# Kernel optimization log

Measured on AMD Instinct MI355X. Metric: run time of the kernel, lower is better.

## Reference

```python
import jax, jax.numpy as jnp
import numpy as np

V, N, D, C = 3, 4096, 512, 10
PSI = 0.7
CE_SCALE = 0.1


def setup_inputs() -> dict:
    key = jax.random.key(0)
    ks = jax.random.split(key, 10)
    X = jax.random.normal(ks[0], (V, N, D), jnp.float32)
    # sparse-ish symmetric binary adjacency per view (dense storage, as in source)
    A = (jax.random.uniform(ks[1], (V, N, N)) < 0.01).astype(jnp.float32)
    A = jnp.maximum(A, jnp.swapaxes(A, 1, 2))
    # ce_scale * Dirichlet(alpha=ones(C)) samples, one per (view, node)
    consensus = CE_SCALE * jax.random.dirichlet(ks[2], jnp.ones((C,), jnp.float32), (V, N)).astype(jnp.float32)
    W_mlp = jax.random.normal(ks[3], (V, D, C), jnp.float32) * 0.05
    b_mlp = jnp.zeros((V, C), jnp.float32)
    W1 = jax.random.normal(ks[4], (V, D, D), jnp.float32) * 0.05
    b1 = jnp.zeros((V, D), jnp.float32)
    W2 = jax.random.normal(ks[5], (V, D, C), jnp.float32) * 0.05
    b2 = jnp.zeros((V, C), jnp.float32)
    return {"X": X, "A": A, "consensus": consensus, "W_mlp": W_mlp, "b_mlp": b_mlp,
            "W1": W1, "b1": b1, "W2": W2, "b2": b2}


def _gcn_norm(A):
    # A: [V, N, N].  A_hat = A + I;  A_norm = D^{-1/2} A_hat D^{-1/2}
    A_hat = A + jnp.eye(A.shape[-1], dtype=A.dtype)
    dinv = 1.0 / jnp.sqrt(jnp.sum(A_hat, axis=-1))          # [V, N]
    return dinv[:, :, None] * A_hat * dinv[:, None, :]


def reference(X, A, consensus, W_mlp, b_mlp, W1, b1, W2, b2):
    # --- EvidenceCollector (single Linear -> Softplus; dropout is eval-identity) ---
    mlp = jax.nn.softplus(jnp.einsum('vnd,vdc->vnc', X, W_mlp) + b_mlp[:, None, :])
    # --- GCN: softplus(gcn2(gcn1(X, A), A)) ---
    A_norm = _gcn_norm(A)                                    # [V, N, N]
    h = jnp.einsum('vij,vjd->vid', A_norm, X)
    h = jnp.einsum('vnd,vde->vne', h, W1) + b1[:, None, :]   # gcn1 linear
    h = jnp.einsum('vij,vjc->vic', A_norm, h)
    gcn = jax.nn.softplus(jnp.einsum('vnd,vdc->vnc', h, W2) + b2[:, None, :])
    E = consensus + mlp + gcn                                # evidences, [V, N, C]

    # --- create_complete_graph: mean cosine similarity per view-pair (i<j) ---
    En = E / jnp.clip(jnp.linalg.norm(E, axis=-1, keepdims=True), 1e-8)
    S = jnp.einsum('inc,jnc->ij', En, En) / E.shape[1]       # [V, V] mean cos-sim
    mask = jnp.triu(jnp.ones((V, V), bool), k=1)             # edges (i, j), i<j
    max_sim = jnp.max(jnp.where(mask, S, -jnp.inf))
    thr = PSI * max_sim
    w = jnp.where(mask & (S > thr), S, 0.0)                  # thresholded weights

    # --- mrf_aggregate: per-source-row softmax over its edges, weighted sum ---
    logits = jnp.where(mask, w, -1e30)
    m = jnp.max(logits, axis=1, keepdims=True)
    e = jnp.exp(logits - m) * mask                           # zero for non-edges
    p = e / jnp.clip(jnp.sum(e, axis=1, keepdims=True), 1e-30)  # empty rows -> 0
    # sum_{i,j>i} p[i,j] * (E[j] + E[i])
    agg = jnp.einsum('ij,jnc->nc', p, E) + jnp.einsum('i,inc->nc', jnp.sum(p, axis=1), E)
    agg = agg / (2.0 * V)
    return (E, agg)
```

## Files before the change

kernel.cpp:

```cpp
#include <hip/hip_runtime.h>
#include <stdint.h>
#include <stddef.h>

#define VV 3
#define NN 4096
#define DD 512
#define CC 10

typedef unsigned short bf16_t;
typedef __attribute__((ext_vector_type(8))) short bf16x8;
typedef __attribute__((ext_vector_type(4))) float f32x4;

#define MFMA16 __builtin_amdgcn_mfma_f32_16x16x32_bf16

__device__ __forceinline__ float bf2f(unsigned u) {
  union { unsigned u; float f; } c; c.u = u << 16; return c.f;
}
__device__ __forceinline__ bf16_t f2bf(float f) {
  union { float f; unsigned u; } c; c.f = f;
  unsigned r = (c.u + 0x7FFFu + ((c.u >> 16) & 1u)) >> 16;
  return (bf16_t)r;
}
__device__ __forceinline__ float splus(float x) {
  float ax = fabsf(x);
  return fmaxf(x, 0.0f) + log1pf(expf(-ax));
}

__global__ __launch_bounds__(256) void k_prep(const float* __restrict__ A,
    const float* __restrict__ W1, const float* __restrict__ b1,
    const float* __restrict__ W2, const float* __restrict__ W_mlp,
    unsigned long long* __restrict__ mask, float* __restrict__ dinv,
    bf16_t* __restrict__ Wc_t, float* __restrict__ bp, bf16_t* __restrict__ Wm_t)
{
  int t = threadIdx.x;
  int w = t >> 6, lane = t & 63;
  if (blockIdx.x < VV * NN / 4) {
    size_t row = (size_t)blockIdx.x * 4 + w;
    const f32x4* r4 = (const f32x4*)(A + row * NN);
    unsigned long long myw = 0ull;
#pragma unroll 8
    for (int it = 0; it < 16; ++it) {
      f32x4 x = __builtin_nontemporal_load(r4 + it * 64 + lane);
      unsigned long long q0 = __ballot(x[0] != 0.0f);
      unsigned long long q1 = __ballot(x[1] != 0.0f);
      unsigned long long q2 = __ballot(x[2] != 0.0f);
      unsigned long long q3 = __ballot(x[3] != 0.0f);
      if ((lane >> 2) == it) {
        int k = lane & 3;
        myw = (k == 0) ? q0 : (k == 1) ? q1 : (k == 2) ? q2 : q3;
      }
    }
    mask[row * 64 + lane] = myw;
    int pc = __popcll(myw);
#pragma unroll
    for (int s = 32; s; s >>= 1) pc += __shfl_xor(pc, s);
    if (lane == 0) dinv[row] = 1.0f / sqrtf((float)(pc + 1));
  } else if (blockIdx.x < VV * NN / 4 + 385) {
    int wid = (blockIdx.x - VV * NN / 4) * 4 + w;
    if (wid >= VV * 513) return;
    int v = wid / 513, dd2 = wid % 513;
    const float* w2 = W2 + (size_t)v * DD * CC;
    const float* src = (dd2 < DD) ? (W1 + ((size_t)v * DD + dd2) * DD) : (b1 + (size_t)v * DD);
    float acc[CC];
#pragma unroll
    for (int c = 0; c < CC; ++c) acc[c] = 0.f;
    for (int it = 0; it < 8; ++it) {
      float wv = src[it * 64 + lane];
      const float* w2r = w2 + (size_t)(it * 64 + lane) * CC;
#pragma unroll
      for (int c = 0; c < CC; ++c) acc[c] += wv * w2r[c];
    }
#pragma unroll
    for (int c = 0; c < CC; ++c) {
#pragma unroll
      for (int s = 32; s; s >>= 1) acc[c] += __shfl_xor(acc[c], s);
    }
    if (lane == 0) {
      if (dd2 < DD) {
#pragma unroll
        for (int c = 0; c < CC; ++c) Wc_t[((size_t)v * 16 + c) * DD + dd2] = f2bf(acc[c]);
#pragma unroll
        for (int c = CC; c < 16; ++c) Wc_t[((size_t)v * 16 + c) * DD + dd2] = 0;
      } else {
#pragma unroll
        for (int c = 0; c < CC; ++c) bp[v * CC + c] = acc[c];
      }
    }
  } else {
    int idx = (blockIdx.x - (VV * NN / 4 + 385)) * 256 + t;
    if (idx >= VV * DD) return;
    int v = idx / DD, d = idx % DD;
#pragma unroll
    for (int c = 0; c < CC; ++c)
      Wm_t[((size_t)v * 16 + c) * DD + d] = f2bf(W_mlp[((size_t)v * DD + d) * CC + c]);
#pragma unroll
    for (int c = CC; c < 16; ++c) Wm_t[((size_t)v * 16 + c) * DD + d] = 0;
  }
}

__global__ __launch_bounds__(256) void k_zs(
    const float* __restrict__ X,
    const bf16_t* __restrict__ Wc_t, const bf16_t* __restrict__ Wm_t,
    const float* __restrict__ b_mlp, const float* __restrict__ consensus,
    const float* __restrict__ dinv,
    unsigned* __restrict__ Ps1p, float* __restrict__ E)
{
  __shared__ bf16_t Bc[16 * 520];
  __shared__ bf16_t Bm[16 * 520];
  int v = blockIdx.y;
  int t = threadIdx.x;
  {
    int r = t & 15, ch = t >> 4;
    const bf16_t* sc = Wc_t + (size_t)v * 16 * DD + (size_t)r * DD + ch * 32;
    const bf16_t* sm = Wm_t + (size_t)v * 16 * DD + (size_t)r * DD + ch * 32;
    bf16_t* dc = &Bc[r * 520 + ch * 32];
    bf16_t* dm = &Bm[r * 520 + ch * 32];
#pragma unroll
    for (int q = 0; q < 4; ++q) {
      *(bf16x8*)(dc + q * 8) = *(const bf16x8*)(sc + q * 8);
      *(bf16x8*)(dm + q * 8) = *(const bf16x8*)(sm + q * 8);
    }
  }
  __syncthreads();
  int w = t >> 6, lane = t & 63;
  int fl = lane & 15, fh = lane >> 4;
  int r0 = blockIdx.x * 64 + w * 16;
  const float* Xrow = X + ((size_t)v * NN + r0 + fl) * DD;
  f32x4 aP = {0.f, 0.f, 0.f, 0.f}, aM = {0.f, 0.f, 0.f, 0.f};
#pragma unroll
  for (int k = 0; k < 16; ++k) {
    float4 x0 = *(const float4*)(Xrow + k * 32 + fh * 8);
    float4 x1 = *(const float4*)(Xrow + k * 32 + fh * 8 + 4);
    bf16x8 a = { (short)f2bf(x0.x), (short)f2bf(x0.y), (short)f2bf(x0.z), (short)f2bf(x0.w),
                 (short)f2bf(x1.x), (short)f2bf(x1.y), (short)f2bf(x1.z), (short)f2bf(x1.w) };
    bf16x8 b1v = *(const bf16x8*)(&Bc[fl * 520 + k * 32 + fh * 8]);
    aP = MFMA16(a, b1v, aP, 0, 0, 0);
    bf16x8 b2v = *(const bf16x8*)(&Bm[fl * 520 + k * 32 + fh * 8]);
    aM = MFMA16(a, b2v, aM, 0, 0, 0);
  }
  float bmv = (fl < CC) ? b_mlp[v * CC + fl] : 0.f;
#pragma unroll
  for (int g = 0; g < 4; ++g) {
    int j = r0 + fh * 4 + g;
    float dj = dinv[(size_t)v * NN + j];
    float val = aP[g] * dj;
    float part = __shfl_xor(val, 1);
    if (((fl & 1) == 0) && fl < CC) {
      unsigned pw = (unsigned)f2bf(val) | ((unsigned)f2bf(part) << 16);
      Ps1p[((size_t)v * 5 + (fl >> 1)) * NN + j] = pw;
    }
    if (fl < CC) {
      size_t ad = ((size_t)v * NN + j) * CC + fl;
      E[ad] = consensus[ad] + splus(aM[g] + bmv);
    }
  }
}

#define SPMM_PROLOG(SRC_) \
  __shared__ unsigned PsL[5 * NN];   \
  int v = blockIdx.y; \
  int t = threadIdx.x; \
  { \
    const uint4* src_ = (const uint4*)((SRC_) + (size_t)v * 5 * NN); \
    uint4* dst_ = (uint4*)PsL; \
    _Pragma("unroll") \
    for (int q = 0; q < 20; ++q) dst_[q * 256 + t] = src_[q * 256 + t]; \
  } \
  __syncthreads(); \
  int w = t >> 6, g = (t >> 3) & 7, s = t & 7; \
  int i = blockIdx.x * 32 + w * 8 + g; \
  const unsigned long long* mrow = mask + ((size_t)v * NN + i) * 64; \
  float acc[CC]; \
  _Pragma("unroll") \
  for (int c = 0; c < CC; ++c) acc[c] = 0.f; \
  _Pragma("unroll") \
  for (int it = 0; it < 8; ++it) { \
    int wi = it * 8 + s; \
    unsigned long long bits = mrow[wi]; \
    int jb = (wi >> 2) * 256 + (wi & 3); \
    while (bits) { \
      int b = __builtin_ctzll(bits); \
      bits &= bits - 1; \
      int j = jb + (b << 2); \
      _Pragma("unroll") \
      for (int c2 = 0; c2 < 5; ++c2) { \
        unsigned pw = PsL[c2 * NN + j]; \
        acc[2 * c2]     += bf2f(pw & 0xFFFFu); \
        acc[2 * c2 + 1] += bf2f(pw >> 16); \
      } \
    } \
  } \
  _Pragma("unroll") \
  for (int c = 0; c < CC; ++c) { \
    acc[c] += __shfl_xor(acc[c], 1); \
    acc[c] += __shfl_xor(acc[c], 2); \
    acc[c] += __shfl_xor(acc[c], 4); \
  }

__global__ __launch_bounds__(256) void k_spmm1(
    const unsigned long long* __restrict__ mask, const unsigned* __restrict__ Ps1p,
    const float* __restrict__ bp, const float* __restrict__ dinv,
    unsigned* __restrict__ P2p)
{
  SPMM_PROLOG(Ps1p)
  if (s == 0) {
    float di = dinv[(size_t)v * NN + i];
#pragma unroll
    for (int c2 = 0; c2 < 5; ++c2) {
      unsigned pw = PsL[c2 * NN + i];
      acc[2 * c2]     += bf2f(pw & 0xFFFFu);
      acc[2 * c2 + 1] += bf2f(pw >> 16);
    }
#pragma unroll
    for (int c2 = 0; c2 < 5; ++c2) {
      float lo = di * (di * acc[2 * c2]     + bp[v * CC + 2 * c2]);
      float hi = di * (di * acc[2 * c2 + 1] + bp[v * CC + 2 * c2 + 1]);
      P2p[((size_t)v * 5 + c2) * NN + i] = (unsigned)f2bf(lo) | ((unsigned)f2bf(hi) << 16);
    }
  }
}

__global__ __launch_bounds__(256) void k_spmm2(
    const unsigned long long* __restrict__ mask, const unsigned* __restrict__ P2p,
    const float* __restrict__ b2, const float* __restrict__ dinv,
    float* __restrict__ E)
{
  SPMM_PROLOG(P2p)
  if (s == 0) {
    float di = dinv[(size_t)v * NN + i];
#pragma unroll
    for (int c2 = 0; c2 < 5; ++c2) {
      unsigned pw = PsL[c2 * NN + i];
      acc[2 * c2]     += bf2f(pw & 0xFFFFu);
      acc[2 * c2 + 1] += bf2f(pw >> 16);
    }
    float* Eo = E + ((size_t)v * NN + i) * CC;
#pragma unroll
    for (int c = 0; c < CC; ++c)
      Eo[c] = Eo[c] + splus(di * acc[c] + b2[v * CC + c]);
  }
}

__global__ __launch_bounds__(256) void k_tail(const float* __restrict__ E,
    float* __restrict__ partial, unsigned* __restrict__ barcnt,
    float* __restrict__ agg)
{
  __shared__ float sm[3][256];
  int t = threadIdx.x;
  int bid = blockIdx.x;
  if (bid < 16) {
    int n = bid * 256 + t;
    float e0[CC], e1[CC], e2[CC];
#pragma unroll
    for (int c = 0; c < CC; ++c) {
      e0[c] = E[(size_t)(0 * NN + n) * CC + c];
      e1[c] = E[(size_t)(1 * NN + n) * CC + c];
      e2[c] = E[(size_t)(2 * NN + n) * CC + c];
    }
    float n0 = 0, n1 = 0, n2 = 0, d01 = 0, d02 = 0, d12 = 0;
#pragma unroll
    for (int c = 0; c < CC; ++c) { n0 += e0[c]*e0[c]; n1 += e1[c]*e1[c]; n2 += e2[c]*e2[c]; }
    float i0 = 1.0f / fmaxf(sqrtf(n0), 1e-8f);
    float i1 = 1.0f / fmaxf(sqrtf(n1), 1e-8f);
    float i2 = 1.0f / fmaxf(sqrtf(n2), 1e-8f);
#pragma unroll
    for (int c = 0; c < CC; ++c) { d01 += e0[c]*e1[c]; d02 += e0[c]*e2[c]; d12 += e1[c]*e2[c]; }
    sm[0][t] = d01 * i0 * i1;
    sm[1][t] = d02 * i0 * i2;
    sm[2][t] = d12 * i1 * i2;
    __syncthreads();
    for (int s = 128; s; s >>= 1) {
      if (t < s) { sm[0][t] += sm[0][t+s]; sm[1][t] += sm[1][t+s]; sm[2][t] += sm[2][t+s]; }
      __syncthreads();
    }
    if (t == 0) {
      partial[bid * 3 + 0] = sm[0][0];
      partial[bid * 3 + 1] = sm[1][0];
      partial[bid * 3 + 2] = sm[2][0];
    }
  }
  __syncthreads();
  if (t == 0) {
    __builtin_amdgcn_fence(__ATOMIC_RELEASE, "agent");
    __hip_atomic_fetch_add(barcnt, 1u, __ATOMIC_RELAXED, __HIP_MEMORY_SCOPE_AGENT);
    while (__hip_atomic_load(barcnt, __ATOMIC_RELAXED, __HIP_MEMORY_SCOPE_AGENT) < 160u)
      __builtin_amdgcn_s_sleep(8);
    __builtin_amdgcn_fence(__ATOMIC_ACQUIRE, "agent");
  }
  __syncthreads();
  float S01 = 0, S02 = 0, S12 = 0;
  for (int b = 0; b < 16; ++b) {
    S01 += partial[b * 3 + 0];
    S02 += partial[b * 3 + 1];
    S12 += partial[b * 3 + 2];
  }
  S01 /= (float)NN; S02 /= (float)NN; S12 /= (float)NN;
  float mx = fmaxf(S01, fmaxf(S02, S12));
  float thr = 0.7f * mx;
  float w01 = (S01 > thr) ? S01 : 0.f;
  float w02 = (S02 > thr) ? S02 : 0.f;
  float m0 = fmaxf(w01, w02);
  float e01 = expf(w01 - m0), e02 = expf(w02 - m0);
  float s0 = e01 + e02;
  float p01 = e01 / s0, p02 = e02 / s0;
  float p12 = 1.0f;
  float c0 = (p01 + p02) / 6.0f;
  float c1 = (p12 + p01) / 6.0f;
  float c2 = (p02 + p12) / 6.0f;
  int idx = bid * 256 + t;
  agg[idx] = c0 * E[idx] + c1 * E[NN * CC + idx] + c2 * E[2 * NN * CC + idx];
}

extern "C" void kernel_launch(void* const* d_in, const int* in_sizes, int n_in,
                              void* d_out, int out_size, void* d_ws, size_t ws_size,
                              hipStream_t stream)
{
  (void)in_sizes; (void)n_in; (void)out_size;
  const float* X         = (const float*)d_in[0];
  const float* A         = (const float*)d_in[1];
  const float* consensus = (const float*)d_in[2];
  const float* W_mlp     = (const float*)d_in[3];
  const float* b_mlp     = (const float*)d_in[4];
  const float* W1        = (const float*)d_in[5];
  const float* b1        = (const float*)d_in[6];
  const float* W2        = (const float*)d_in[7];
  const float* b2        = (const float*)d_in[8];
  float* Eout = (float*)d_out;
  float* aggout = Eout + (size_t)VV * NN * CC;

  char* ws = (char*)d_ws;
  size_t off = 0;
  auto alloc = [&](size_t b) { char* p = ws + off; off += (b + 255) & ~(size_t)255; return p; };
  unsigned long long* mask = (unsigned long long*)alloc((size_t)VV * NN * 64 * 8);
  bf16_t* Wc_t  = (bf16_t*)alloc((size_t)VV * 16 * DD * 2);
  bf16_t* Wm_t  = (bf16_t*)alloc((size_t)VV * 16 * DD * 2);
  float*  bp    = (float*) alloc((size_t)VV * CC * 4);
  float*  dinv  = (float*) alloc((size_t)VV * NN * 4);
  unsigned* Ps1p = (unsigned*)alloc((size_t)VV * 5 * NN * 4);
  unsigned* P2p  = (unsigned*)alloc((size_t)VV * 5 * NN * 4);
  float*  partial = (float*)alloc(16 * 3 * 4);
  unsigned* barcnt = (unsigned*)alloc(256);
  if (off > ws_size) return;

  hipMemsetAsync(barcnt, 0, 4, stream);
  k_prep <<<VV * NN / 4 + 385 + 6, 256, 0, stream>>>(A, W1, b1, W2, W_mlp,
                                                     mask, dinv, Wc_t, bp, Wm_t);
  k_zs   <<<dim3(NN / 64, VV), 256, 0, stream>>>(X, Wc_t, Wm_t, b_mlp, consensus,
                                                 dinv, Ps1p, Eout);
  k_spmm1<<<dim3(NN / 32, VV), 256, 0, stream>>>(mask, Ps1p, bp, dinv, P2p);
  k_spmm2<<<dim3(NN / 32, VV), 256, 0, stream>>>(mask, P2p, b2, dinv, Eout);
  k_tail <<<160, 256, 0, stream>>>(Eout, partial, barcnt, aggout);
}
```

Measured before the change: 97.15 us.

## Fuse all stages into one cooperative persistent kernel with grid barriers

Replaces five separate launches with one cooperative kernel of 512 blocks that runs the stages prep, projection, two SpMM passes, similarity and aggregation, separated by atomic grid barriers. The intent is to remove inter-kernel launch gaps. The SpMM gathers now read directly from a node-major padded P layout (8 words per node) in global memory instead of staging the whole per-view P array into LDS. The adjacency scan is spread over fewer blocks, each handling 6 rows per wave, and no longer uses nontemporal loads. The risks are lower parallelism in the 50 MB adjacency scan, barrier spin cost, and uncached gather traffic. If the cooperative launch fails, the code falls back to six separate launches.

```diff
diff --git a/kernel.cpp b/kernel.cpp
--- a/kernel.cpp
+++ b/kernel.cpp
@@ -6,6 +6,7 @@
 #define NN 4096
 #define DD 512
 #define CC 10
+#define NBLK 512
 
 typedef unsigned short bf16_t;
 typedef __attribute__((ext_vector_type(8))) short bf16x8;
@@ -26,21 +27,73 @@
   return fmaxf(x, 0.0f) + log1pf(expf(-ax));
 }
 
-__global__ __launch_bounds__(256) void k_prep(const float* __restrict__ A,
-    const float* __restrict__ W1, const float* __restrict__ b1,
-    const float* __restrict__ W2, const float* __restrict__ W_mlp,
+__device__ __forceinline__ void gsync(unsigned* cnt, unsigned target, int t) {
+  __syncthreads();
+  if (t == 0) {
+    __builtin_amdgcn_fence(__ATOMIC_RELEASE, "agent");
+    __hip_atomic_fetch_add(cnt, 1u, __ATOMIC_RELAXED, __HIP_MEMORY_SCOPE_AGENT);
+    while (__hip_atomic_load(cnt, __ATOMIC_RELAXED, __HIP_MEMORY_SCOPE_AGENT) < target)
+      __builtin_amdgcn_s_sleep(16);
+    __builtin_amdgcn_fence(__ATOMIC_ACQUIRE, "agent");
+  }
+  __syncthreads();
+}
+
+__device__ __forceinline__ void dev_prep(int bid, int t,
+    const float* __restrict__ A, const float* __restrict__ W1,
+    const float* __restrict__ b1, const float* __restrict__ W2,
+    const float* __restrict__ W_mlp,
     unsigned long long* __restrict__ mask, float* __restrict__ dinv,
     bf16_t* __restrict__ Wc_t, float* __restrict__ bp, bf16_t* __restrict__ Wm_t)
 {
-  int t = threadIdx.x;
   int w = t >> 6, lane = t & 63;
-  if (blockIdx.x < VV * NN / 4) {
-    size_t row = (size_t)blockIdx.x * 4 + w;
+  int gw = bid * 4 + w;
+  int gt = bid * 256 + t;
+  if (gt < VV * DD) {
+    int v = gt / DD, d = gt - v * DD;
+#pragma unroll
+    for (int c = 0; c < CC; ++c)
+      Wm_t[((size_t)v * 16 + c) * DD + d] = f2bf(W_mlp[((size_t)v * DD + d) * CC + c]);
+#pragma unroll
+    for (int c = CC; c < 16; ++c) Wm_t[((size_t)v * 16 + c) * DD + d] = 0;
+  }
+  if (gw < VV * 513) {
+    int v = gw / 513, dd2 = gw % 513;
+    const float* w2 = W2 + (size_t)v * DD * CC;
+    const float* src = (dd2 < DD) ? (W1 + ((size_t)v * DD + dd2) * DD) : (b1 + (size_t)v * DD);
+    float acc[CC];
+#pragma unroll
+    for (int c = 0; c < CC; ++c) acc[c] = 0.f;
+    for (int it = 0; it < 8; ++it) {
+      float wv = src[it * 64 + lane];
+      const float* w2r = w2 + (size_t)(it * 64 + lane) * CC;
+#pragma unroll
+      for (int c = 0; c < CC; ++c) acc[c] += wv * w2r[c];
+    }
+#pragma unroll
+    for (int c = 0; c < CC; ++c) {
+#pragma unroll
+      for (int s = 32; s; s >>= 1) acc[c] += __shfl_xor(acc[c], s);
+    }
+    if (lane == 0) {
+      if (dd2 < DD) {
+#pragma unroll
+        for (int c = 0; c < CC; ++c) Wc_t[((size_t)v * 16 + c) * DD + dd2] = f2bf(acc[c]);
+#pragma unroll
+        for (int c = CC; c < 16; ++c) Wc_t[((size_t)v * 16 + c) * DD + dd2] = 0;
+      } else {
+#pragma unroll
+        for (int c = 0; c < CC; ++c) bp[v * CC + c] = acc[c];
+      }
+    }
+  }
+  for (int p = 0; p < 6; ++p) {
+    size_t row = (size_t)gw * 6 + p;
     const f32x4* r4 = (const f32x4*)(A + row * NN);
     unsigned long long myw = 0ull;
-#pragma unroll 8
+#pragma unroll 4
     for (int it = 0; it < 16; ++it) {
-      f32x4 x = __builtin_nontemporal_load(r4 + it * 64 + lane);
+      f32x4 x = r4[it * 64 + lane];
       unsigned long long q0 = __ballot(x[0] != 0.0f);
       unsigned long long q1 = __ballot(x[1] != 0.0f);
       unsigned long long q2 = __ballot(x[2] != 0.0f);
@@ -55,76 +108,33 @@
 #pragma unroll
     for (int s = 32; s; s >>= 1) pc += __shfl_xor(pc, s);
     if (lane == 0) dinv[row] = 1.0f / sqrtf((float)(pc + 1));
-  } else if (blockIdx.x < VV * NN / 4 + 385) {
-    int wid = (blockIdx.x - VV * NN / 4) * 4 + w;
-    if (wid >= VV * 513) return;
-    int v = wid / 513, dd2 = wid % 513;
-    const float* w2 = W2 + (size_t)v * DD * CC;
-    const float* src = (dd2 < DD) ? (W1 + ((size_t)v * DD + dd2) * DD) : (b1 + (size_t)v * DD);
-    float acc[CC];
-#pragma unroll
-    for (int c = 0; c < CC; ++c) acc[c] = 0.f;
-    for (int it = 0; it < 8; ++it) {
-      float wv = src[it * 64 + lane];
-      const float* w2r = w2 + (size_t)(it * 64 + lane) * CC;
-#pragma unroll
-      for (int c = 0; c < CC; ++c) acc[c] += wv * w2r[c];
-    }
-#pragma unroll
-    for (int c = 0; c < CC; ++c) {
-#pragma unroll
-      for (int s = 32; s; s >>= 1) acc[c] += __shfl_xor(acc[c], s);
-    }
-    if (lane == 0) {
-      if (dd2 < DD) {
-#pragma unroll
-        for (int c = 0; c < CC; ++c) Wc_t[((size_t)v * 16 + c) * DD + dd2] = f2bf(acc[c]);
-#pragma unroll
-        for (int c = CC; c < 16; ++c) Wc_t[((size_t)v * 16 + c) * DD + dd2] = 0;
-      } else {
-#pragma unroll
-        for (int c = 0; c < CC; ++c) bp[v * CC + c] = acc[c];
-      }
-    }
-  } else {
-    int idx = (blockIdx.x - (VV * NN / 4 + 385)) * 256 + t;
-    if (idx >= VV * DD) return;
-    int v = idx / DD, d = idx % DD;
-#pragma unroll
-    for (int c = 0; c < CC; ++c)
-      Wm_t[((size_t)v * 16 + c) * DD + d] = f2bf(W_mlp[((size_t)v * DD + d) * CC + c]);
-#pragma unroll
-    for (int c = CC; c < 16; ++c) Wm_t[((size_t)v * 16 + c) * DD + d] = 0;
-  }
-}
-
-__global__ __launch_bounds__(256) void k_zs(
-    const float* __restrict__ X,
-    const bf16_t* __restrict__ Wc_t, const bf16_t* __restrict__ Wm_t,
-    const float* __restrict__ b_mlp, const float* __restrict__ consensus,
-    const float* __restrict__ dinv,
+  }
+}
+
+__device__ __forceinline__ void dev_zs(int bid, int t, bf16_t* Bc, bf16_t* Bm,
+    const float* __restrict__ X, const bf16_t* __restrict__ Wc_t,
+    const bf16_t* __restrict__ Wm_t, const float* __restrict__ b_mlp,
+    const float* __restrict__ consensus, const float* __restrict__ dinv,
     unsigned* __restrict__ Ps1p, float* __restrict__ E)
 {
-  __shared__ bf16_t Bc[16 * 520];
-  __shared__ bf16_t Bm[16 * 520];
-  int v = blockIdx.y;
-  int t = threadIdx.x;
+  if (bid >= 192) return;
+  int v = bid / 64, xb = bid % 64;
   {
     int r = t & 15, ch = t >> 4;
     const bf16_t* sc = Wc_t + (size_t)v * 16 * DD + (size_t)r * DD + ch * 32;
-    const bf16_t* sm = Wm_t + (size_t)v * 16 * DD + (size_t)r * DD + ch * 32;
+    const bf16_t* sm2 = Wm_t + (size_t)v * 16 * DD + (size_t)r * DD + ch * 32;
     bf16_t* dc = &Bc[r * 520 + ch * 32];
     bf16_t* dm = &Bm[r * 520 + ch * 32];
 #pragma unroll
     for (int q = 0; q < 4; ++q) {
       *(bf16x8*)(dc + q * 8) = *(const bf16x8*)(sc + q * 8);
-      *(bf16x8*)(dm + q * 8) = *(const bf16x8*)(sm + q * 8);
+      *(bf16x8*)(dm + q * 8) = *(const bf16x8*)(sm2 + q * 8);
     }
   }
   __syncthreads();
   int w = t >> 6, lane = t & 63;
   int fl = lane & 15, fh = lane >> 4;
-  int r0 = blockIdx.x * 64 + w * 16;
+  int r0 = xb * 64 + w * 16;
   const float* Xrow = X + ((size_t)v * NN + r0 + fl) * DD;
   f32x4 aP = {0.f, 0.f, 0.f, 0.f}, aM = {0.f, 0.f, 0.f, 0.f};
 #pragma unroll
@@ -147,7 +157,7 @@
     float part = __shfl_xor(val, 1);
     if (((fl & 1) == 0) && fl < CC) {
       unsigned pw = (unsigned)f2bf(val) | ((unsigned)f2bf(part) << 16);
-      Ps1p[((size_t)v * 5 + (fl >> 1)) * NN + j] = pw;
+      Ps1p[((size_t)v * NN + j) * 8 + (fl >> 1)] = pw;
     }
     if (fl < CC) {
       size_t ad = ((size_t)v * NN + j) * CC + fl;
@@ -156,138 +166,114 @@
   }
 }
 
-#define SPMM_PROLOG(SRC_) \
-  __shared__ unsigned PsL[5 * NN];   \
-  int v = blockIdx.y; \
-  int t = threadIdx.x; \
-  { \
-    const uint4* src_ = (const uint4*)((SRC_) + (size_t)v * 5 * NN); \
-    uint4* dst_ = (uint4*)PsL; \
-    _Pragma("unroll") \
-    for (int q = 0; q < 20; ++q) dst_[q * 256 + t] = src_[q * 256 + t]; \
-  } \
-  __syncthreads(); \
-  int w = t >> 6, g = (t >> 3) & 7, s = t & 7; \
-  int i = blockIdx.x * 32 + w * 8 + g; \
-  const unsigned long long* mrow = mask + ((size_t)v * NN + i) * 64; \
-  float acc[CC]; \
-  _Pragma("unroll") \
-  for (int c = 0; c < CC; ++c) acc[c] = 0.f; \
-  _Pragma("unroll") \
-  for (int it = 0; it < 8; ++it) { \
-    int wi = it * 8 + s; \
-    unsigned long long bits = mrow[wi]; \
-    int jb = (wi >> 2) * 256 + (wi & 3); \
-    while (bits) { \
-      int b = __builtin_ctzll(bits); \
-      bits &= bits - 1; \
-      int j = jb + (b << 2); \
-      _Pragma("unroll") \
-      for (int c2 = 0; c2 < 5; ++c2) { \
-        unsigned pw = PsL[c2 * NN + j]; \
-        acc[2 * c2]     += bf2f(pw & 0xFFFFu); \
-        acc[2 * c2 + 1] += bf2f(pw >> 16); \
-      } \
-    } \
-  } \
-  _Pragma("unroll") \
-  for (int c = 0; c < CC; ++c) { \
-    acc[c] += __shfl_xor(acc[c], 1); \
-    acc[c] += __shfl_xor(acc[c], 2); \
-    acc[c] += __shfl_xor(acc[c], 4); \
-  }
-
-__global__ __launch_bounds__(256) void k_spmm1(
-    const unsigned long long* __restrict__ mask, const unsigned* __restrict__ Ps1p,
-    const float* __restrict__ bp, const float* __restrict__ dinv,
-    unsigned* __restrict__ P2p)
-{
-  SPMM_PROLOG(Ps1p)
-  if (s == 0) {
-    float di = dinv[(size_t)v * NN + i];
-#pragma unroll
-    for (int c2 = 0; c2 < 5; ++c2) {
-      unsigned pw = PsL[c2 * NN + i];
-      acc[2 * c2]     += bf2f(pw & 0xFFFFu);
-      acc[2 * c2 + 1] += bf2f(pw >> 16);
-    }
-#pragma unroll
-    for (int c2 = 0; c2 < 5; ++c2) {
-      float lo = di * (di * acc[2 * c2]     + bp[v * CC + 2 * c2]);
-      float hi = di * (di * acc[2 * c2 + 1] + bp[v * CC + 2 * c2 + 1]);
-      P2p[((size_t)v * 5 + c2) * NN + i] = (unsigned)f2bf(lo) | ((unsigned)f2bf(hi) << 16);
-    }
-  }
-}
-
-__global__ __launch_bounds__(256) void k_spmm2(
-    const unsigned long long* __restrict__ mask, const unsigned* __restrict__ P2p,
-    const float* __restrict__ b2, const float* __restrict__ dinv,
-    float* __restrict__ E)
-{
-  SPMM_PROLOG(P2p)
-  if (s == 0) {
-    float di = dinv[(size_t)v * NN + i];
-#pragma unroll
-    for (int c2 = 0; c2 < 5; ++c2) {
-      unsigned pw = PsL[c2 * NN + i];
-      acc[2 * c2]     += bf2f(pw & 0xFFFFu);
-      acc[2 * c2 + 1] += bf2f(pw >> 16);
-    }
-    float* Eo = E + ((size_t)v * NN + i) * CC;
-#pragma unroll
-    for (int c = 0; c < CC; ++c)
-      Eo[c] = Eo[c] + splus(di * acc[c] + b2[v * CC + c]);
-  }
-}
-
-__global__ __launch_bounds__(256) void k_tail(const float* __restrict__ E,
-    float* __restrict__ partial, unsigned* __restrict__ barcnt,
+template<int PASS>
+__device__ __forceinline__ void dev_spmm(int bid, int t,
+    const unsigned long long* __restrict__ mask, const unsigned* __restrict__ Pin,
+    const float* __restrict__ bvec, const float* __restrict__ dinv,
+    unsigned* __restrict__ Pout, float* __restrict__ E)
+{
+  int gid = (bid * 256 + t) >> 3;
+  int s8 = t & 7;
+  if (gid >= VV * NN) return;
+  int v = gid >> 12;
+  const unsigned long long* mrow = mask + (size_t)gid * 64;
+  const unsigned* Pv = Pin + (size_t)v * NN * 8;
+  float acc[CC];
+#pragma unroll
+  for (int c = 0; c < CC; ++c) acc[c] = 0.f;
+#pragma unroll
+  for (int it = 0; it < 8; ++it) {
+    int wi = it * 8 + s8;
+    unsigned long long bits = mrow[wi];
+    int jb = (wi >> 2) * 256 + (wi & 3);
+    while (bits) {
+      int b = __builtin_ctzll(bits);
+      bits &= bits - 1;
+      int j = jb + (b << 2);
+      const unsigned* pw = Pv + (size_t)j * 8;
+      uint4 p0 = *(const uint4*)pw;
+      unsigned p4 = pw[4];
+      acc[0] += bf2f(p0.x & 0xFFFFu); acc[1] += bf2f(p0.x >> 16);
+      acc[2] += bf2f(p0.y & 0xFFFFu); acc[3] += bf2f(p0.y >> 16);
+      acc[4] += bf2f(p0.z & 0xFFFFu); acc[5] += bf2f(p0.z >> 16);
+      acc[6] += bf2f(p0.w & 0xFFFFu); acc[7] += bf2f(p0.w >> 16);
+      acc[8] += bf2f(p4 & 0xFFFFu);   acc[9] += bf2f(p4 >> 16);
+    }
+  }
+#pragma unroll
+  for (int c = 0; c < CC; ++c) {
+    acc[c] += __shfl_xor(acc[c], 1);
+    acc[c] += __shfl_xor(acc[c], 2);
+    acc[c] += __shfl_xor(acc[c], 4);
+  }
+  if (s8 == 0) {
+    const unsigned* ps = Pin + (size_t)gid * 8;
+    uint4 p0 = *(const uint4*)ps;
+    unsigned p4 = ps[4];
+    acc[0] += bf2f(p0.x & 0xFFFFu); acc[1] += bf2f(p0.x >> 16);
+    acc[2] += bf2f(p0.y & 0xFFFFu); acc[3] += bf2f(p0.y >> 16);
+    acc[4] += bf2f(p0.z & 0xFFFFu); acc[5] += bf2f(p0.z >> 16);
+    acc[6] += bf2f(p0.w & 0xFFFFu); acc[7] += bf2f(p0.w >> 16);
+    acc[8] += bf2f(p4 & 0xFFFFu);   acc[9] += bf2f(p4 >> 16);
+    float di = dinv[gid];
+    if (PASS == 1) {
+#pragma unroll
+      for (int c2 = 0; c2 < 5; ++c2) {
+        float lo = di * (di * acc[2 * c2]     + bvec[v * CC + 2 * c2]);
+        float hi = di * (di * acc[2 * c2 + 1] + bvec[v * CC + 2 * c2 + 1]);
+        Pout[(size_t)gid * 8 + c2] = (unsigned)f2bf(lo) | ((unsigned)f2bf(hi) << 16);
+      }
+    } else {
+      float* Eo = E + (size_t)gid * CC;
+#pragma unroll
+      for (int c = 0; c < CC; ++c)
+        Eo[c] = Eo[c] + splus(di * acc[c] + bvec[v * CC + c]);
+    }
+  }
+}
+
+__device__ __forceinline__ void dev_sim(int bid, int t, float* sm,
+    const float* __restrict__ E, float* __restrict__ partial)
+{
+  if (bid >= 16) return;
+  int n = bid * 256 + t;
+  float e0[CC], e1[CC], e2[CC];
+#pragma unroll
+  for (int c = 0; c < CC; ++c) {
+    e0[c] = E[(size_t)(0 * NN + n) * CC + c];
+    e1[c] = E[(size_t)(1 * NN + n) * CC + c];
+    e2[c] = E[(size_t)(2 * NN + n) * CC + c];
+  }
+  float n0 = 0, n1 = 0, n2 = 0, d01 = 0, d02 = 0, d12 = 0;
+#pragma unroll
+  for (int c = 0; c < CC; ++c) { n0 += e0[c]*e0[c]; n1 += e1[c]*e1[c]; n2 += e2[c]*e2[c]; }
+  float i0 = 1.0f / fmaxf(sqrtf(n0), 1e-8f);
+  float i1 = 1.0f / fmaxf(sqrtf(n1), 1e-8f);
+  float i2 = 1.0f / fmaxf(sqrtf(n2), 1e-8f);
+#pragma unroll
+  for (int c = 0; c < CC; ++c) { d01 += e0[c]*e1[c]; d02 += e0[c]*e2[c]; d12 += e1[c]*e2[c]; }
+  sm[0 * 256 + t] = d01 * i0 * i1;
+  sm[1 * 256 + t] = d02 * i0 * i2;
+  sm[2 * 256 + t] = d12 * i1 * i2;
+  __syncthreads();
+  for (int s = 128; s; s >>= 1) {
+    if (t < s) {
+      sm[0*256+t] += sm[0*256+t+s]; sm[1*256+t] += sm[1*256+t+s]; sm[2*256+t] += sm[2*256+t+s];
+    }
+    __syncthreads();
+  }
+  if (t == 0) {
+    partial[bid * 3 + 0] = sm[0];
+    partial[bid * 3 + 1] = sm[256];
+    partial[bid * 3 + 2] = sm[512];
+  }
+}
+
+__device__ __forceinline__ void dev_agg(int bid, int t,
+    const float* __restrict__ E, const float* __restrict__ partial,
     float* __restrict__ agg)
 {
-  __shared__ float sm[3][256];
-  int t = threadIdx.x;
-  int bid = blockIdx.x;
-  if (bid < 16) {
-    int n = bid * 256 + t;
-    float e0[CC], e1[CC], e2[CC];
-#pragma unroll
-    for (int c = 0; c < CC; ++c) {
-      e0[c] = E[(size_t)(0 * NN + n) * CC + c];
-      e1[c] = E[(size_t)(1 * NN + n) * CC + c];
-      e2[c] = E[(size_t)(2 * NN + n) * CC + c];
-    }
-    float n0 = 0, n1 = 0, n2 = 0, d01 = 0, d02 = 0, d12 = 0;
-#pragma unroll
-    for (int c = 0; c < CC; ++c) { n0 += e0[c]*e0[c]; n1 += e1[c]*e1[c]; n2 += e2[c]*e2[c]; }
-    float i0 = 1.0f / fmaxf(sqrtf(n0), 1e-8f);
-    float i1 = 1.0f / fmaxf(sqrtf(n1), 1e-8f);
-    float i2 = 1.0f / fmaxf(sqrtf(n2), 1e-8f);
-#pragma unroll
-    for (int c = 0; c < CC; ++c) { d01 += e0[c]*e1[c]; d02 += e0[c]*e2[c]; d12 += e1[c]*e2[c]; }
-    sm[0][t] = d01 * i0 * i1;
-    sm[1][t] = d02 * i0 * i2;
-    sm[2][t] = d12 * i1 * i2;
-    __syncthreads();
-    for (int s = 128; s; s >>= 1) {
-      if (t < s) { sm[0][t] += sm[0][t+s]; sm[1][t] += sm[1][t+s]; sm[2][t] += sm[2][t+s]; }
-      __syncthreads();
-    }
-    if (t == 0) {
-      partial[bid * 3 + 0] = sm[0][0];
-      partial[bid * 3 + 1] = sm[1][0];
-      partial[bid * 3 + 2] = sm[2][0];
-    }
-  }
-  __syncthreads();
-  if (t == 0) {
-    __builtin_amdgcn_fence(__ATOMIC_RELEASE, "agent");
-    __hip_atomic_fetch_add(barcnt, 1u, __ATOMIC_RELAXED, __HIP_MEMORY_SCOPE_AGENT);
-    while (__hip_atomic_load(barcnt, __ATOMIC_RELAXED, __HIP_MEMORY_SCOPE_AGENT) < 160u)
-      __builtin_amdgcn_s_sleep(8);
-    __builtin_amdgcn_fence(__ATOMIC_ACQUIRE, "agent");
-  }
-  __syncthreads();
+  if (bid >= 160) return;
   float S01 = 0, S02 = 0, S12 = 0;
   for (int b = 0; b < 16; ++b) {
     S01 += partial[b * 3 + 0];
@@ -311,6 +297,55 @@
   agg[idx] = c0 * E[idx] + c1 * E[NN * CC + idx] + c2 * E[2 * NN * CC + idx];
 }
 
+__global__ __launch_bounds__(256) void k_all(
+    const float* __restrict__ A, const float* __restrict__ X,
+    const float* __restrict__ consensus,
+    const float* __restrict__ W_mlp, const float* __restrict__ b_mlp,
+    const float* __restrict__ W1, const float* __restrict__ b1,
+    const float* __restrict__ W2, const float* __restrict__ b2,
+    unsigned long long* __restrict__ mask,
+    bf16_t* __restrict__ Wc_t, bf16_t* __restrict__ Wm_t, float* __restrict__ bp,
+    float* __restrict__ dinv, unsigned* __restrict__ Ps1p,
+    unsigned* __restrict__ P2p, float* __restrict__ partial,
+    unsigned* __restrict__ barcnt, float* __restrict__ E, float* __restrict__ agg)
+{
+  __shared__ bf16_t Bc[16 * 520];
+  __shared__ bf16_t Bm[16 * 520];
+  __shared__ float sm[3 * 256];
+  int t = threadIdx.x, bid = blockIdx.x;
+  dev_prep(bid, t, A, W1, b1, W2, W_mlp, mask, dinv, Wc_t, bp, Wm_t);
+  gsync(barcnt, 1 * NBLK, t);
+  dev_zs(bid, t, Bc, Bm, X, Wc_t, Wm_t, b_mlp, consensus, dinv, Ps1p, E);
+  gsync(barcnt, 2 * NBLK, t);
+  dev_spmm<1>(bid, t, mask, Ps1p, bp, dinv, P2p, E);
+  gsync(barcnt, 3 * NBLK, t);
+  dev_spmm<2>(bid, t, mask, P2p, b2, dinv, (unsigned*)nullptr, E);
+  gsync(barcnt, 4 * NBLK, t);
+  dev_sim(bid, t, sm, E, partial);
+  gsync(barcnt, 5 * NBLK, t);
+  dev_agg(bid, t, E, partial, agg);
+}
+
+__global__ __launch_bounds__(256) void k_one(int ph,
+    const float* A, const float* X, const float* consensus,
+    const float* W_mlp, const float* b_mlp,
+    const float* W1, const float* b1, const float* W2, const float* b2,
+    unsigned long long* mask, bf16_t* Wc_t, bf16_t* Wm_t, float* bp,
+    float* dinv, unsigned* Ps1p, unsigned* P2p, float* partial,
+    float* E, float* agg)
+{
+  __shared__ bf16_t Bc[16 * 520];
+  __shared__ bf16_t Bm[16 * 520];
+  __shared__ float sm[3 * 256];
+  int t = threadIdx.x, bid = blockIdx.x;
+  if (ph == 0)      dev_prep(bid, t, A, W1, b1, W2, W_mlp, mask, dinv, Wc_t, bp, Wm_t);
+  else if (ph == 1) dev_zs(bid, t, Bc, Bm, X, Wc_t, Wm_t, b_mlp, consensus, dinv, Ps1p, E);
+  else if (ph == 2) dev_spmm<1>(bid, t, mask, Ps1p, bp, dinv, P2p, E);
+  else if (ph == 3) dev_spmm<2>(bid, t, mask, P2p, b2, dinv, (unsigned*)nullptr, E);
+  else if (ph == 4) dev_sim(bid, t, sm, E, partial);
+  else              dev_agg(bid, t, E, partial, agg);
+}
+
 extern "C" void kernel_launch(void* const* d_in, const int* in_sizes, int n_in,
                               void* d_out, int out_size, void* d_ws, size_t ws_size,
                               hipStream_t stream)
@@ -336,18 +371,35 @@
   bf16_t* Wm_t  = (bf16_t*)alloc((size_t)VV * 16 * DD * 2);
   float*  bp    = (float*) alloc((size_t)VV * CC * 4);
   float*  dinv  = (float*) alloc((size_t)VV * NN * 4);
-  unsigned* Ps1p = (unsigned*)alloc((size_t)VV * 5 * NN * 4);
-  unsigned* P2p  = (unsigned*)alloc((size_t)VV * 5 * NN * 4);
+  unsigned* Ps1p = (unsigned*)alloc((size_t)VV * NN * 8 * 4);
+  unsigned* P2p  = (unsigned*)alloc((size_t)VV * NN * 8 * 4);
   float*  partial = (float*)alloc(16 * 3 * 4);
   unsigned* barcnt = (unsigned*)alloc(256);
   if (off > ws_size) return;
 
   hipMemsetAsync(barcnt, 0, 4, stream);
-  k_prep <<<VV * NN / 4 + 385 + 6, 256, 0, stream>>>(A, W1, b1, W2, W_mlp,
-                                                     mask, dinv, Wc_t, bp, Wm_t);
-  k_zs   <<<dim3(NN / 64, VV), 256, 0, stream>>>(X, Wc_t, Wm_t, b_mlp, consensus,
-                                                 dinv, Ps1p, Eout);
-  k_spmm1<<<dim3(NN / 32, VV), 256, 0, stream>>>(mask, Ps1p, bp, dinv, P2p);
-  k_spmm2<<<dim3(NN / 32, VV), 256, 0, stream>>>(mask, P2p, b2, dinv, Eout);
-  k_tail <<<160, 256, 0, stream>>>(Eout, partial, barcnt, aggout);
-}
+
+  void* kargs[] = {
+    (void*)&A, (void*)&X, (void*)&consensus, (void*)&W_mlp, (void*)&b_mlp,
+    (void*)&W1, (void*)&b1, (void*)&W2, (void*)&b2,
+    (void*)&mask, (void*)&Wc_t, (void*)&Wm_t, (void*)&bp, (void*)&dinv,
+    (void*)&Ps1p, (void*)&P2p, (void*)&partial, (void*)&barcnt,
+    (void*)&Eout, (void*)&aggout
+  };
+  hipError_t err = hipLaunchCooperativeKernel((const void*)k_all, dim3(NBLK),
+                                              dim3(256), kargs, 0, stream);
+  if (err != hipSuccess) {
+    k_one<<<NBLK, 256, 0, stream>>>(0, A, X, consensus, W_mlp, b_mlp, W1, b1, W2, b2,
+                                    mask, Wc_t, Wm_t, bp, dinv, Ps1p, P2p, partial, Eout, aggout);
+    k_one<<<192, 256, 0, stream>>>(1, A, X, consensus, W_mlp, b_mlp, W1, b1, W2, b2,
+                                   mask, Wc_t, Wm_t, bp, dinv, Ps1p, P2p, partial, Eout, aggout);
+    k_one<<<NBLK, 256, 0, stream>>>(2, A, X, consensus, W_mlp, b_mlp, W1, b1, W2, b2,
+                                    mask, Wc_t, Wm_t, bp, dinv, Ps1p, P2p, partial, Eout, aggout);
+    k_one<<<NBLK, 256, 0, stream>>>(3, A, X, consensus, W_mlp, b_mlp, W1, b1, W2, b2,
+                                    mask, Wc_t, Wm_t, bp, dinv, Ps1p, P2p, partial, Eout, aggout);
+    k_one<<<16, 256, 0, stream>>>(4, A, X, consensus, W_mlp, b_mlp, W1, b1, W2, b2,
+                                  mask, Wc_t, Wm_t, bp, dinv, Ps1p, P2p, partial, Eout, aggout);
+    k_one<<<160, 256, 0, stream>>>(5, A, X, consensus, W_mlp, b_mlp, W1, b1, W2, b2,
+                                   mask, Wc_t, Wm_t, bp, dinv, Ps1p, P2p, partial, Eout, aggout);
+  }
+}
```

New measurement: 289.1 us. +197.6%, slower.
